# Kernel tuning notes

Hardware: AMD Instinct MI355X
Metric: run time of the kernel (lower is better)

Reference implementation:

```python
import jax, jax.numpy as jnp
import numpy as np
from jax import lax

S, B = 2048, 2048          # seq_len, batch (seq-first layout like nn.LSTM)
IN, H, OUT, L = 2, 4, 1, 4  # from module defaults


def setup_inputs() -> dict:
    key = jax.random.key(0)
    ks = jax.random.split(key, 11)
    s = 0.5  # ~ PyTorch init scale 1/sqrt(H)
    return {
        "x": jax.random.normal(ks[0], (S, B, IN), jnp.float32),
        "W_ih0": jax.random.normal(ks[1], (4 * H, IN), jnp.float32) * s,
        "W_hh0": jax.random.normal(ks[2], (4 * H, H), jnp.float32) * s,
        "b_ih0": jax.random.normal(ks[3], (4 * H,), jnp.float32) * s,
        "b_hh0": jax.random.normal(ks[4], (4 * H,), jnp.float32) * s,
        "W_ihr": jax.random.normal(ks[5], (L - 1, 4 * H, H), jnp.float32) * s,
        "W_hhr": jax.random.normal(ks[6], (L - 1, 4 * H, H), jnp.float32) * s,
        "b_ihr": jax.random.normal(ks[7], (L - 1, 4 * H), jnp.float32) * s,
        "b_hhr": jax.random.normal(ks[8], (L - 1, 4 * H), jnp.float32) * s,
        "W_out": jax.random.normal(ks[9], (OUT, H), jnp.float32) * s,
        "b_out": jax.random.normal(ks[10], (OUT,), jnp.float32) * s,
    }


def _lstm_layer(x, Wih, Whh, b):
    # x: [S, B, D_in]; PyTorch gate order: i, f, g, o
    Bsz = x.shape[1]
    Hh = Whh.shape[1]
    # precompute input contribution for all timesteps (batched GEMM)
    xg = jnp.einsum('sbd,gd->sbg', x, Wih) + b  # [S, B, 4H]

    def step(carry, xgt):
        h, c = carry
        gates = xgt + h @ Whh.T  # [B, 4H]
        i, f, g, o = jnp.split(gates, 4, axis=-1)
        c = jax.nn.sigmoid(f) * c + jax.nn.sigmoid(i) * jnp.tanh(g)
        h = jax.nn.sigmoid(o) * jnp.tanh(c)
        return (h, c), h

    init = (jnp.zeros((Bsz, Hh), x.dtype), jnp.zeros((Bsz, Hh), x.dtype))
    _, ys = lax.scan(step, init, xg)
    return ys  # [S, B, H]


def reference(x, W_ih0, W_hh0, b_ih0, b_hh0, W_ihr, W_hhr, b_ihr, b_hhr, W_out, b_out):
    h = _lstm_layer(x, W_ih0, W_hh0, b_ih0 + b_hh0)
    for l in range(W_ihr.shape[0]):  # fixed small layer loop
        h = _lstm_layer(h, W_ihr[l], W_hhr[l], b_ihr[l] + b_hhr[l])
    # dropout: identity in eval mode (deterministic reference)
    y = jnp.einsum('sbh,oh->sbo', h, W_out) + b_out  # linear head, [S, B, 1]
    return y
```

## Files before the change

kernel.cpp:

```cpp
#include <hip/hip_runtime.h>

#define S_LEN 2048
#define B_SZ 2048

typedef float v2 __attribute__((ext_vector_type(2)));
#define FMA2(a, b, c) __builtin_elementwise_fma((a), (b), (c))

template <int CTRL>
__device__ __forceinline__ float dppmov(float v) {
  int r = __builtin_amdgcn_update_dpp(0, __builtin_bit_cast(int, v), CTRL, 0xF,
                                      0xF, true);
  return __builtin_bit_cast(float, r);
}

#define TICK(U)                                                                \
  {                                                                            \
                \
    float s0 = dppmov<0x114>(hv01.x);                           \
    float s1 = dppmov<0x114>(hv01.y);                                          \
    float s2 = dppmov<0x114>(hv23.x);                                          \
    float s3 = dppmov<0x114>(hv23.y);                                          \
    v2 h01, h23;                                                               \
    h01.x = hx0;                                                               \
    h01.y = hx1;                                                               \
    h23.x = hx2;                                                               \
    h23.y = hx3;                                                               \
    v2 A0 = FMA2(wi01[0], h01, bias2[0]);                                      \
    v2 A1 = FMA2(wi01[1], h01, bias2[1]);                                      \
    v2 A2 = FMA2(wi01[2], h01, bias2[2]);                                      \
    v2 A3 = FMA2(wi01[3], h01, bias2[3]);                                      \
    A0 = FMA2(wi23[0], h23, A0);                                               \
    A1 = FMA2(wi23[1], h23, A1);                                               \
    A2 = FMA2(wi23[2], h23, A2);                                               \
    A3 = FMA2(wi23[3], h23, A3);                                               \
    A0 = FMA2(wh01[0], hv01, A0);                                              \
    A1 = FMA2(wh01[1], hv01, A1);                                              \
    A2 = FMA2(wh01[2], hv01, A2);                                              \
    A3 = FMA2(wh01[3], hv01, A3);                                              \
    A0 = FMA2(wh23[0], hv23, A0);                                              \
    A1 = FMA2(wh23[1], hv23, A1);                                              \
    A2 = FMA2(wh23[2], hv23, A2);                                              \
    A3 = FMA2(wh23[3], hv23, A3);                                              \
    float a0 = A0.x + A0.y, a1 = A1.x + A1.y;                                  \
    float a2 = A2.x + A2.y, a3 = A3.x + A3.y;                                  \
    float e0 = __builtin_amdgcn_exp2f(a0);       \
    float e1 = __builtin_amdgcn_exp2f(a1);                                     \
    float e2 = __builtin_amdgcn_exp2f(a2);                                     \
    float e3 = __builtin_amdgcn_exp2f(a3);                                     \
    float r0 = __builtin_amdgcn_rcpf(1.0f + e0);               \
    float r1 = __builtin_amdgcn_rcpf(1.0f + e1);               \
    float r2 = __builtin_amdgcn_rcpf(1.0f + e2);            \
    float r3 = __builtin_amdgcn_rcpf(1.0f + e3);               \
    float gi = KT * r0;                               \
    float gg = fmaf(2.0f, r2, -1.0f);                             \
    cKT = fmaf(r1, cKT, gi * gg);                                              \
    float te = __builtin_amdgcn_exp2f(cKT);                                    \
    float tr = __builtin_amdgcn_rcpf(1.0f + te);                               \
    float go2 = r3 + r3;                                                       \
    float hh = fmaf(go2, tr, -r3);                          \
    hv01.x = hh;                                                               \
    hv01.y = dppmov<0x39>(hh);                                \
    hv23.x = dppmov<0x4E>(hh);                                \
    hv23.y = dppmov<0x93>(hh);                                \
           \
           \
    hx0 = lz ? xc##U.x : s0;                                                   \
    hx1 = lz ? xc##U.y : s1;                                                   \
    hx2 = s2;                                                                  \
    hx3 = s3;                                                                  \
             \
    float yv = fmaf(wo3, hv23.y,                                               \
                    fmaf(wo2, hv23.x, fmaf(wo1, hv01.y, fmaf(wo0, hv01.x,      \
                                                             bo))));           \
    if (yl && (unsigned)ty < (unsigned)S_LEN) outp[yi] = yv;                   \
    ty += 1;                                                                   \
    yi += B_SZ;                                                                \
  }

#define RESET(U)                                                               \
  if (2 * l > (U)) {                                                           \
    cKT = 0.0f;                                                                \
    hv01.x = 0.0f;                                                             \
    hv01.y = 0.0f;                                                             \
    hv23.x = 0.0f;                                                             \
    hv23.y = 0.0f;                                                             \
  }

#define XLOAD(U, TB)                                                           \
  {                                                                            \
    int t_ = (TB) + (U);                                                       \
    if (t_ >= S_LEN) t_ = S_LEN - 1;          \
    xc##U = px[(size_t)t_ * B_SZ + bidx];                                      \
  }

__global__ void __launch_bounds__(64, 1)
    lstm_kernel(const float *__restrict__ x, const float *__restrict__ Wih0,
                const float *__restrict__ Whh0, const float *__restrict__ bih0,
                const float *__restrict__ bhh0, const float *__restrict__ Wihr,
                const float *__restrict__ Whhr, const float *__restrict__ bihr,
                const float *__restrict__ bhhr, const float *__restrict__ Wout,
                const float *__restrict__ bout, float *__restrict__ out) {
  const int lane = threadIdx.x & 63;
  const int b = lane >> 4;
  const int l = (lane >> 2) & 3;
  const int j = lane & 3;
  const int bidx = blockIdx.x * 4 + b;
  const bool lz = (l == 0);
  const bool yl = (l == 3) && (j == 0);

  const float L2E = 1.4426950408889634f;
  const float KT = -2.8853900817779268f;
  const float kks[4] = {-L2E, -L2E, -2.0f * L2E, -L2E};

  v2 wi01[4], wi23[4], wh01[4], wh23[4], bias2[4];
#pragma unroll
  for (int t = 0; t < 4; ++t) {
    const int row = t * 4 + j;
    const float kk = kks[t];
    float i0, i1, i2, i3, w0, w1, w2, w3, bs;
    if (l == 0) {
      i0 = Wih0[row * 2 + 0];
      i1 = Wih0[row * 2 + 1];
      i2 = 0.0f;
      i3 = 0.0f;
      w0 = Whh0[row * 4 + j];
      w1 = Whh0[row * 4 + ((j + 1) & 3)];
      w2 = Whh0[row * 4 + ((j + 2) & 3)];
      w3 = Whh0[row * 4 + ((j + 3) & 3)];
      bs = bih0[row] + bhh0[row];
    } else {
      const int m = l - 1;
      i0 = Wihr[m * 64 + row * 4 + j];
      i1 = Wihr[m * 64 + row * 4 + ((j + 1) & 3)];
      i2 = Wihr[m * 64 + row * 4 + ((j + 2) & 3)];
      i3 = Wihr[m * 64 + row * 4 + ((j + 3) & 3)];
      w0 = Whhr[m * 64 + row * 4 + j];
      w1 = Whhr[m * 64 + row * 4 + ((j + 1) & 3)];
      w2 = Whhr[m * 64 + row * 4 + ((j + 2) & 3)];
      w3 = Whhr[m * 64 + row * 4 + ((j + 3) & 3)];
      bs = bihr[m * 16 + row] + bhhr[m * 16 + row];
    }
    wi01[t].x = kk * i0;
    wi01[t].y = kk * i1;
    wi23[t].x = kk * i2;
    wi23[t].y = kk * i3;
    wh01[t].x = kk * w0;
    wh01[t].y = kk * w1;
    wh23[t].x = kk * w2;
    wh23[t].y = kk * w3;
    bias2[t].x = kk * bs;
    bias2[t].y = 0.0f;
  }
  const float wo0 = Wout[0], wo1 = Wout[1], wo2 = Wout[2], wo3 = Wout[3];
  const float bo = bout[0];

  const float2 *__restrict__ px = (const float2 *)x;
  float *__restrict__ outp = out;

  v2 hv01, hv23;
  hv01.x = 0.0f;
  hv01.y = 0.0f;
  hv23.x = 0.0f;
  hv23.y = 0.0f;
  float cKT = 0.0f;
  float hx0, hx1, hx2, hx3;

  {
    float2 x00 = px[bidx];
    hx0 = lz ? x00.x : 0.0f;
    hx1 = lz ? x00.y : 0.0f;
    hx2 = 0.0f;
    hx3 = 0.0f;
  }

  float2 xc0 = px[1 * B_SZ + bidx];
  float2 xc1 = px[2 * B_SZ + bidx];
  float2 xc2 = px[3 * B_SZ + bidx];
  float2 xc3 = px[4 * B_SZ + bidx];
  float2 xc4 = px[5 * B_SZ + bidx];
  float2 xc5 = px[6 * B_SZ + bidx];
  float2 xc6 = px[7 * B_SZ + bidx];
  float2 xc7 = px[8 * B_SZ + bidx];

  int ty = -6;
  int yi = -6 * B_SZ + bidx;

  TICK(0); RESET(0); XLOAD(0, 9);
  TICK(1); RESET(1); XLOAD(1, 9);
  TICK(2); RESET(2); XLOAD(2, 9);
  TICK(3); RESET(3); XLOAD(3, 9);
  TICK(4); RESET(4); XLOAD(4, 9);
  TICK(5); RESET(5); XLOAD(5, 9);
  TICK(6); XLOAD(6, 9);
  TICK(7); XLOAD(7, 9);

#pragma unroll 1
  for (int k = 1; k < 257; ++k) {
    const int tb = 8 * k + 9;
    TICK(0); XLOAD(0, tb);
    TICK(1); XLOAD(1, tb);
    TICK(2); XLOAD(2, tb);
    TICK(3); XLOAD(3, tb);
    TICK(4); XLOAD(4, tb);
    TICK(5); XLOAD(5, tb);
    TICK(6); XLOAD(6, tb);
    TICK(7); XLOAD(7, tb);
  }
}

extern "C" void kernel_launch(void *const *d_in, const int *in_sizes, int n_in,
                              void *d_out, int out_size, void *d_ws,
                              size_t ws_size, hipStream_t stream) {
  (void)in_sizes;
  (void)n_in;
  (void)out_size;
  (void)d_ws;
  (void)ws_size;
  const float *x = (const float *)d_in[0];
  const float *Wih0 = (const float *)d_in[1];
  const float *Whh0 = (const float *)d_in[2];
  const float *bih0 = (const float *)d_in[3];
  const float *bhh0 = (const float *)d_in[4];
  const float *Wihr = (const float *)d_in[5];
  const float *Whhr = (const float *)d_in[6];
  const float *bihr = (const float *)d_in[7];
  const float *bhhr = (const float *)d_in[8];
  const float *Wout = (const float *)d_in[9];
  const float *bout = (const float *)d_in[10];
  lstm_kernel<<<dim3(B_SZ / 4), dim3(64), 0, stream>>>(
      x, Wih0, Whh0, bih0, bhh0, Wihr, Whhr, bihr, bhhr, Wout, bout,
      (float *)d_out);
}
```

Baseline: 437.3 us.

## Fold layer-0 input select into DPP old value and batch output stores

Uses the DPP old-value operand (bound_ctrl off) so lanes with no source row keep the new x input or zero, which removes the per-tick select on the layer index. Output projections are buffered in registers as packed FMAs, and each group of eight steps is stored together under a single branch. The loop is restructured with pointer increments, a peeled prologue and epilogue, and no per-step bounds checks. The aim is fewer scalar and vector instructions on the serial recurrence's critical path. The cost is more registers held for the eight buffered outputs.

```diff
diff --git a/kernel.cpp b/kernel.cpp
--- a/kernel.cpp
+++ b/kernel.cpp
@@ -13,13 +13,21 @@
   return __builtin_bit_cast(float, r);
 }
 
+template <int CTRL, bool BC>
+__device__ __forceinline__ float dppold(float old, float v) {
+  int r = __builtin_amdgcn_update_dpp(__builtin_bit_cast(int, old),
+                                      __builtin_bit_cast(int, v), CTRL, 0xF,
+                                      0xF, BC);
+  return __builtin_bit_cast(float, r);
+}
+
 #define TICK(U)                                                                \
   {                                                                            \
-                \
-    float s0 = dppmov<0x114>(hv01.x);                           \
-    float s1 = dppmov<0x114>(hv01.y);                                          \
-    float s2 = dppmov<0x114>(hv23.x);                                          \
-    float s3 = dppmov<0x114>(hv23.y);                                          \
+            \
+    float ns0 = dppold<0x114, false>(xc##U.x, hv01.x);          \
+    float ns1 = dppold<0x114, false>(xc##U.y, hv01.y);                         \
+    float ns2 = dppold<0x114, true>(0.0f, hv23.x);                             \
+    float ns3 = dppold<0x114, true>(0.0f, hv23.y);                             \
     v2 h01, h23;                                                               \
     h01.x = hx0;                                                               \
     h01.y = hx1;                                                               \
@@ -62,19 +70,13 @@
     hv01.y = dppmov<0x39>(hh);                                \
     hv23.x = dppmov<0x4E>(hh);                                \
     hv23.y = dppmov<0x93>(hh);                                \
-           \
-           \
-    hx0 = lz ? xc##U.x : s0;                                                   \
-    hx1 = lz ? xc##U.y : s1;                                                   \
-    hx2 = s2;                                                                  \
-    hx3 = s3;                                                                  \
              \
-    float yv = fmaf(wo3, hv23.y,                                               \
-                    fmaf(wo2, hv23.x, fmaf(wo1, hv01.y, fmaf(wo0, hv01.x,      \
-                                                             bo))));           \
-    if (yl && (unsigned)ty < (unsigned)S_LEN) outp[yi] = yv;                   \
-    ty += 1;                                                                   \
-    yi += B_SZ;                                                                \
+    y##U = FMA2(wo01v, hv01, bo2);                                             \
+    y##U = FMA2(wo23v, hv23, y##U);                                            \
+    hx0 = ns0;                                                                 \
+    hx1 = ns1;                                                                 \
+    hx2 = ns2;                                                                 \
+    hx3 = ns3;                                                                 \
   }
 
 #define RESET(U)                                                               \
@@ -86,12 +88,10 @@
     hv23.y = 0.0f;                                                             \
   }
 
-#define XLOAD(U, TB)                                                           \
-  {                                                                            \
-    int t_ = (TB) + (U);                                                       \
-    if (t_ >= S_LEN) t_ = S_LEN - 1;          \
-    xc##U = px[(size_t)t_ * B_SZ + bidx];                                      \
-  }
+#define XLOAD(U) xc##U = pxk[(U)*B_SZ];
+#define XLOAD7C xc7 = pxk[6 * B_SZ];
+
+#define YST(U) ypk[(U)*B_SZ] = y##U.x + y##U.y;
 
 __global__ void __launch_bounds__(64, 1)
     lstm_kernel(const float *__restrict__ x, const float *__restrict__ Wih0,
@@ -151,11 +151,15 @@
     bias2[t].x = kk * bs;
     bias2[t].y = 0.0f;
   }
-  const float wo0 = Wout[0], wo1 = Wout[1], wo2 = Wout[2], wo3 = Wout[3];
-  const float bo = bout[0];
+  v2 wo01v, wo23v, bo2;
+  wo01v.x = Wout[0];
+  wo01v.y = Wout[1];
+  wo23v.x = Wout[2];
+  wo23v.y = Wout[3];
+  bo2.x = bout[0];
+  bo2.y = 0.0f;
 
   const float2 *__restrict__ px = (const float2 *)x;
-  float *__restrict__ outp = out;
 
   v2 hv01, hv23;
   hv01.x = 0.0f;
@@ -164,6 +168,7 @@
   hv23.y = 0.0f;
   float cKT = 0.0f;
   float hx0, hx1, hx2, hx3;
+  v2 y0, y1, y2, y3, y4, y5, y6, y7;
 
   {
     float2 x00 = px[bidx];
@@ -182,29 +187,75 @@
   float2 xc6 = px[7 * B_SZ + bidx];
   float2 xc7 = px[8 * B_SZ + bidx];
 
-  int ty = -6;
-  int yi = -6 * B_SZ + bidx;
-
-  TICK(0); RESET(0); XLOAD(0, 9);
-  TICK(1); RESET(1); XLOAD(1, 9);
-  TICK(2); RESET(2); XLOAD(2, 9);
-  TICK(3); RESET(3); XLOAD(3, 9);
-  TICK(4); RESET(4); XLOAD(4, 9);
-  TICK(5); RESET(5); XLOAD(5, 9);
-  TICK(6); XLOAD(6, 9);
-  TICK(7); XLOAD(7, 9);
+  const float2 *__restrict__ pxk = px + 9 * B_SZ + bidx;
+  float *__restrict__ ypk;
+
+  TICK(0); RESET(0); XLOAD(0);
+  TICK(1); RESET(1); XLOAD(1);
+  TICK(2); RESET(2); XLOAD(2);
+  TICK(3); RESET(3); XLOAD(3);
+  TICK(4); RESET(4); XLOAD(4);
+  TICK(5); RESET(5); XLOAD(5);
+  TICK(6); XLOAD(6);
+  TICK(7); XLOAD(7);
+  if (yl) {
+    out[bidx] = y6.x + y6.y;
+    out[B_SZ + bidx] = y7.x + y7.y;
+  }
+  pxk += 8 * B_SZ;
+  ypk = out + 2 * B_SZ + bidx;
 
 #pragma unroll 1
-  for (int k = 1; k < 257; ++k) {
-    const int tb = 8 * k + 9;
-    TICK(0); XLOAD(0, tb);
-    TICK(1); XLOAD(1, tb);
-    TICK(2); XLOAD(2, tb);
-    TICK(3); XLOAD(3, tb);
-    TICK(4); XLOAD(4, tb);
-    TICK(5); XLOAD(5, tb);
-    TICK(6); XLOAD(6, tb);
-    TICK(7); XLOAD(7, tb);
+  for (int k = 1; k < 254; ++k) {
+    TICK(0); XLOAD(0);
+    TICK(1); XLOAD(1);
+    TICK(2); XLOAD(2);
+    TICK(3); XLOAD(3);
+    TICK(4); XLOAD(4);
+    TICK(5); XLOAD(5);
+    TICK(6); XLOAD(6);
+    TICK(7); XLOAD(7);
+    if (yl) {
+      YST(0); YST(1); YST(2); YST(3); YST(4); YST(5); YST(6); YST(7);
+    }
+    pxk += 8 * B_SZ;
+    ypk += 8 * B_SZ;
+  }
+
+  TICK(0); XLOAD(0);
+  TICK(1); XLOAD(1);
+  TICK(2); XLOAD(2);
+  TICK(3); XLOAD(3);
+  TICK(4); XLOAD(4);
+  TICK(5); XLOAD(5);
+  TICK(6); XLOAD(6);
+  TICK(7); XLOAD7C;
+  if (yl) {
+    YST(0); YST(1); YST(2); YST(3); YST(4); YST(5); YST(6); YST(7);
+  }
+  ypk += 8 * B_SZ;
+
+  TICK(0);
+  TICK(1);
+  TICK(2);
+  TICK(3);
+  TICK(4);
+  TICK(5);
+  TICK(6);
+  TICK(7);
+  if (yl) {
+    YST(0); YST(1); YST(2); YST(3); YST(4); YST(5); YST(6); YST(7);
+  }
+  ypk += 8 * B_SZ;
+
+  TICK(0);
+  TICK(1);
+  TICK(2);
+  TICK(3);
+  TICK(4);
+  TICK(5);
+  if (yl) {
+    YST(0); YST(1); YST(2); YST(3); YST(4); YST(5);
   }
 }
 
```

Measured after the change: 366.4 us. -16.2%, faster.
